# Optimization experiments

Measured on AMD Instinct MI355X. Metric: run time of the kernel, lower is better.

## Reference

```python
import jax, jax.numpy as jnp
import numpy as np

# Sizes derived from init_kwargs via calc_mlp_features:
# total_param=2117777, router_ratio=0.002 -> router_param=4235.554, expert_param=264192
# expert_hidden = 256, router_hidden = 352
N = 131072      # number of coordinate points
CIN = 3         # expert_insize == router_insize (xyz coords)
E = 8           # num_experts
K = 2           # top_k
H = 256         # expert_hidden (also SIREN data_channel)
RH = 352        # router_hidden
NHID = 3        # expert_layers - 2 hidden SIREN layers
W0C = 30.0      # sine frequency w0


def setup_inputs() -> dict:
    key = jax.random.key(0)
    ks = jax.random.split(key, 16)
    u = lambda k, shape, a: jax.random.uniform(k, shape, jnp.float32, -a, a)
    x = jax.random.uniform(ks[0], (N, CIN), jnp.float32, -1.0, 1.0)
    context = jax.random.uniform(ks[1], (N, CIN), jnp.float32, -1.0, 1.0)
    # Router: kaiming-normal weights, torch-default uniform biases
    Wr1 = jax.random.normal(ks[2], (CIN, RH), jnp.float32) * np.float32(np.sqrt(2.0 / CIN))
    br1 = u(ks[3], (RH,), 1.0 / np.sqrt(CIN))
    Wr2 = jax.random.normal(ks[4], (RH, E), jnp.float32) * np.float32(np.sqrt(2.0 / RH))
    br2 = u(ks[5], (E,), 1.0 / np.sqrt(RH))
    # SIREN experts (stacked over E): first layer U(-1/in, 1/in), rest U(+-sqrt(6/in)/30)
    sb = np.sqrt(6.0 / H) / 30.0
    W0 = u(ks[6], (E, CIN, H), 1.0 / CIN)
    b0 = u(ks[7], (E, H), 1.0 / np.sqrt(CIN))
    Wh = u(ks[8], (E, NHID, H, H), sb)
    bh = u(ks[9], (E, NHID, H), 1.0 / np.sqrt(H))
    Wo = u(ks[10], (E, H, H), sb)
    bo = u(ks[11], (E, H), 1.0 / np.sqrt(H))
    # Decoder: Linear(H,H)+ReLU+Linear(H,1)
    Wd1 = jax.random.normal(ks[12], (H, H), jnp.float32) * np.float32(np.sqrt(2.0 / H))
    bd1 = u(ks[13], (H,), 1.0 / np.sqrt(H))
    Wd2 = jax.random.normal(ks[14], (H, 1), jnp.float32) * np.float32(np.sqrt(2.0 / H))
    bd2 = u(ks[15], (1,), 1.0 / np.sqrt(H))
    return dict(x=x, context=context, Wr1=Wr1, br1=br1, Wr2=Wr2, br2=br2,
                W0=W0, b0=b0, Wh=Wh, bh=bh, Wo=Wo, bo=bo,
                Wd1=Wd1, bd1=bd1, Wd2=Wd2, bd2=bd2)


def reference(x, context, Wr1, br1, Wr2, br2, W0, b0, Wh, bh, Wo, bo, Wd1, bd1, Wd2, bd2):
    n = x.shape[0]
    # --- NoisyTopkRouter (eval path: no noise) ---
    logits = jnp.maximum(context @ Wr1 + br1, 0.0) @ Wr2 + br2          # [N, E]
    topv, topi = jax.lax.top_k(logits, K)                                # [N, K]
    # softmax over -inf-filled sparse logits == softmax over the top-k values
    w = jax.nn.softmax(topv, axis=-1)                                    # [N, K]
    gating = jnp.zeros_like(logits).at[jnp.arange(n)[:, None], topi].set(w)  # [N, E], zero off top-k
    # --- Per-expert SIREN, weighted combine ---
    # Masked dispatch + scatter-add in the original equals dense weighted sum
    # because gating is exactly zero for non-selected experts.
    def expert_step(acc, p):
        W0e, b0e, Whe, bhe, Woe, boe, ge = p
        h = jnp.sin(W0C * (x @ W0e + b0e))                # [N, H]
        for i in range(NHID):
            h = jnp.sin(W0C * (h @ Whe[i] + bhe[i]))
        out = h @ Woe + boe                               # [N, H], no output activation
        return acc + out * ge[:, None], None
    acc0 = jnp.zeros((n, H), dtype=x.dtype)
    final, _ = jax.lax.scan(expert_step, acc0, (W0, b0, Wh, bh, Wo, bo, gating.T))
    # --- Decoder ---
    return jnp.maximum(final @ Wd1 + bd1, 0.0) @ Wd2 + bd2               # [N, 1]
```

## Files before the change

kernel.cpp:

```cpp
#include <hip/hip_runtime.h>
#include <stdint.h>

#define N_PTS 131072
#define RH    352
#define BM    256
#define BME   64
#define TPB   512
#define SREV  4.774648292756860f

typedef short  bf16x8 __attribute__((ext_vector_type(8)));
typedef float  f32x16 __attribute__((ext_vector_type(16)));

__device__ __forceinline__ unsigned short f2bf(float f) {
  uint32_t u = __builtin_bit_cast(uint32_t, f);
  u = (u + 0x7FFFu + ((u >> 16) & 1u)) >> 16;
  return (unsigned short)u;
}
__device__ __forceinline__ float bf2f(unsigned short s) {
  return __builtin_bit_cast(float, ((uint32_t)s) << 16);
}
__device__ __forceinline__ float vsin1(float x) {
  float xf = x - floorf(x);
  float r;
  asm("v_sin_f32 %0, %1" : "=v"(r) : "v"(xf));
  return r;
}
__device__ __forceinline__ void ldsload16(const void* g, void* ldsWaveBase) {
  typedef __attribute__((address_space(3))) uint8_t lds_b;
  typedef __attribute__((address_space(1))) uint8_t glob_b;
  __builtin_amdgcn_global_load_lds((const glob_b*)g, (lds_b*)ldsWaveBase, 16, 0, 0);
}
__device__ __forceinline__ f32x16 mfma_bf16(bf16x8 a, bf16x8 b, f32x16 c) {
  return __builtin_amdgcn_mfma_f32_32x32x16_bf16(a, b, c, 0, 0, 0);
}

#define AWLOAD(d0, d1, addr64) \
  asm volatile("global_load_dwordx4 %0, %2, off\n\t" \
               "global_load_dwordx4 %1, %2, off offset:1024" \
               : "=&v"(d0), "=&v"(d1) : "v"(addr64))

#define VWAIT(N, r0, r1) \
  asm volatile("s_waitcnt vmcnt(" #N ")" : "+v"(r0), "+v"(r1))

__global__ __launch_bounds__(512) void pack_kernel(
    const float* __restrict__ W0, const float* __restrict__ b0,
    const float* __restrict__ Wh, const float* __restrict__ bh,
    const float* __restrict__ Wo, const float* __restrict__ bo,
    const float* __restrict__ Wd1, const float* __restrict__ bd1,
    short* __restrict__ pW0, short* __restrict__ pWh,
    short* __restrict__ pWo, short* __restrict__ pWd1)
{
  int b = blockIdx.x, tid = threadIdx.x;
  int jb = tid >> 6, l = tid & 63;
  int j  = jb*32 + (l & 31);
  int s0 = (l >> 5) * 8;
  unsigned short o[8];
  short* dp;

  if (b < 544) {
    int m = b / 17, slice = b % 17;
    int e = m >> 2, t = m & 3;
    const float* src; const float* bias; float scale; short* dst;
    if (t < 3) { src = Wh + (size_t)(e*3+t)*65536; bias = bh + (size_t)(e*3+t)*256; scale = SREV; dst = pWh + (size_t)(e*3+t)*69632; }
    else       { src = Wo + (size_t)e*65536;       bias = bo + (size_t)e*256;       scale = 1.0f; dst = pWo + (size_t)e*69632; }
    if (slice < 16) {
      #pragma unroll
      for (int i = 0; i < 8; ++i) {
        int k = slice*16 + s0 + i;
        o[i] = f2bf(scale * src[(size_t)k*256 + j]);
      }
    } else {
      #pragma unroll
      for (int i = 0; i < 8; ++i) o[i] = 0;
      if (s0 == 0) {
        float a = scale * bias[j];
        unsigned short h = f2bf(a);
        o[0] = h; o[1] = f2bf(a - bf2f(h));
      }
    }
    dp = dst + (size_t)slice*4096 + jb*512 + l*8;
  } else if (b < 552) {
    int e = b - 544;
    const float* w0 = W0 + (size_t)e*768;
    const float* bb = b0 + (size_t)e*256;
    #pragma unroll
    for (int i = 0; i < 8; ++i) {
      int s = s0 + i;
      unsigned short v = 0;
      if (s < 3) v = f2bf(SREV * w0[(size_t)s*256 + j]);
      else if (s < 6) { float a = SREV * w0[(size_t)(s-3)*256 + j]; unsigned short h = f2bf(a); v = f2bf(a - bf2f(h)); }
      else if (s < 9) v = f2bf(SREV * w0[(size_t)(s-6)*256 + j]);
      else if (s == 9)  v = f2bf(SREV * bb[j]);
      else if (s == 10) { float a = SREV * bb[j]; unsigned short h = f2bf(a); v = f2bf(a - bf2f(h)); }
      o[i] = v;
    }
    dp = pW0 + (size_t)e*4096 + jb*512 + l*8;
  } else {
    int slice = b - 552;
    if (slice < 16) {
      #pragma unroll
      for (int i = 0; i < 8; ++i) {
        int k = slice*16 + s0 + i;
        o[i] = f2bf(Wd1[(size_t)k*256 + j]);
      }
    } else {
      #pragma unroll
      for (int i = 0; i < 8; ++i) o[i] = 0;
      if (s0 == 0) {
        float a = bd1[j];
        unsigned short h = f2bf(a);
        o[0] = h; o[1] = f2bf(a - bf2f(h));
      }
    }
    dp = pWd1 + (size_t)slice*4096 + jb*512 + l*8;
  }
  uint4 v;
  v.x = (uint32_t)o[0] | ((uint32_t)o[1] << 16);
  v.y = (uint32_t)o[2] | ((uint32_t)o[3] << 16);
  v.z = (uint32_t)o[4] | ((uint32_t)o[5] << 16);
  v.w = (uint32_t)o[6] | ((uint32_t)o[7] << 16);
  *(uint4*)dp = v;
}

__global__ __launch_bounds__(256) void router_kernel(
    const float* __restrict__ ctx, const float* __restrict__ Wr1,
    const float* __restrict__ br1, const float* __restrict__ Wr2,
    const float* __restrict__ br2, uint4* __restrict__ topk,
    uint32_t* __restrict__ counts)
{
  __shared__ double w1d[RH*4];
  __shared__ double w2d[RH*8];
  __shared__ uint32_t lcnt[8];
  int tid = threadIdx.x;
  for (int i = tid; i < RH; i += 256) {
    w1d[i*4+0] = (double)Wr1[i];
    w1d[i*4+1] = (double)Wr1[352 + i];
    w1d[i*4+2] = (double)Wr1[704 + i];
    w1d[i*4+3] = (double)br1[i];
  }
  for (int i = tid; i < RH*8; i += 256) w2d[i] = (double)Wr2[i];
  if (tid < 8) lcnt[tid] = 0;
  __syncthreads();

  int n = blockIdx.x*256 + tid;
  double c0 = (double)ctx[(size_t)n*3+0];
  double c1 = (double)ctx[(size_t)n*3+1];
  double c2 = (double)ctx[(size_t)n*3+2];
  double lg[8];
  #pragma unroll
  for (int e = 0; e < 8; ++e) lg[e] = (double)br2[e];
  for (int j = 0; j < RH; ++j) {
    const double* a = &w1d[j*4];
    double h = c0*a[0] + c1*a[1] + c2*a[2] + a[3];
    h = h > 0.0 ? h : 0.0;
    const double* bq = &w2d[j*8];
    lg[0] += h*bq[0]; lg[1] += h*bq[1]; lg[2] += h*bq[2]; lg[3] += h*bq[3];
    lg[4] += h*bq[4]; lg[5] += h*bq[5]; lg[6] += h*bq[6]; lg[7] += h*bq[7];
  }
  double v0 = -1e300, v1 = -1e300; int i0 = 0, i1 = 0;
  #pragma unroll
  for (int e = 0; e < 8; ++e) {
    double lv = lg[e];
    if (lv > v0)      { v1 = v0; i1 = i0; v0 = lv; i0 = e; }
    else if (lv > v1) { v1 = lv; i1 = e; }
  }
  float ex = __expf((float)(v1 - v0));
  float s = 1.0f / (1.0f + ex);
  uint4 t;
  t.x = (uint32_t)i0 | ((uint32_t)i1 << 8);
  t.y = __builtin_bit_cast(uint32_t, s);
  t.z = __builtin_bit_cast(uint32_t, ex * s);
  t.w = 0;
  topk[n] = t;
  atomicAdd(&lcnt[i0], 1u); atomicAdd(&lcnt[i1], 1u);
  __syncthreads();
  if (tid < 8) atomicAdd(&counts[tid], lcnt[tid]);
}

__global__ void scan_kernel(const uint32_t* __restrict__ counts,
                            uint32_t* __restrict__ offsets,
                            uint32_t* __restrict__ cursors)
{
  if (threadIdx.x == 0) {
    uint32_t o = 0;
    for (int e = 0; e < 8; ++e) { offsets[e] = o; cursors[e] = o; o += counts[e]; }
    offsets[8] = o;
  }
}

__global__ __launch_bounds__(256) void scatter_kernel(
    const uint4* __restrict__ topk, uint32_t* __restrict__ cursors,
    uint32_t* __restrict__ plist, float* __restrict__ pw)
{
  __shared__ uint32_t lc[8], lb[8];
  int tid = threadIdx.x;
  if (tid < 8) lc[tid] = 0;
  __syncthreads();
  int n = blockIdx.x*256 + tid;
  uint4 t = topk[n];
  uint32_t e0 = t.x & 255u, e1 = (t.x >> 8) & 255u;
  uint32_t p0 = atomicAdd(&lc[e0], 1u);
  uint32_t p1 = atomicAdd(&lc[e1], 1u);
  __syncthreads();
  if (tid < 8) lb[tid] = atomicAdd(&cursors[tid], lc[tid]);
  __syncthreads();
  uint32_t d0 = lb[e0] + p0, d1 = lb[e1] + p1;
  plist[d0] = ((uint32_t)n << 1);      pw[d0] = __builtin_bit_cast(float, t.y);
  plist[d1] = ((uint32_t)n << 1) | 1u; pw[d1] = __builtin_bit_cast(float, t.z);
}

__global__ __launch_bounds__(256, 3) void expert_kernel(
    const float* __restrict__ x, const uint32_t* __restrict__ counts,
    const uint32_t* __restrict__ offsets, const uint32_t* __restrict__ plist,
    const float* __restrict__ pw, const short* __restrict__ pW0,
    const short* __restrict__ pWh, const short* __restrict__ pWo,
    short* __restrict__ outbuf)
{
  __shared__ __align__(16) uint8_t smem[34816];
  uint8_t* hB = smem;
  uint8_t* xB = smem + 32768;

  int tid = threadIdx.x;
  int lane = tid & 63;
  int jq = tid >> 6;
  int aoff = jq*2048 + lane*16;

  bf16x8 bbias;
  #pragma unroll
  for (int i = 0; i < 8; ++i) bbias[i] = 0;
  if (lane < 32) { bbias[0] = (short)0x3F80; bbias[1] = (short)0x3F80; }

  bf16x8 aw[5][2];
  f32x16 acc[2][2];

  int rr = tid >> 2;
  int rq = tid & 3;

  uint32_t tt = blockIdx.x;
  int e = -1; uint32_t cnt = 0;
  #pragma unroll 1
  for (int ee = 0; ee < 8; ++ee) {
    uint32_t c = counts[ee];
    uint32_t nt = (c + (BME-1)) >> 6;
    if (tt < nt) { e = ee; cnt = c; break; }
    tt -= nt;
  }
  if (e < 0) return;
  uint32_t base = offsets[e] + (tt << 6);
  int nvalid = (int)cnt - (int)(tt << 6); if (nvalid > BME) nvalid = BME;

  uint64_t matp[4];
  matp[0] = (uint64_t)(uintptr_t)(pWh + (size_t)(e*3+0)*69632);
  matp[1] = (uint64_t)(uintptr_t)(pWh + (size_t)(e*3+1)*69632);
  matp[2] = (uint64_t)(uintptr_t)(pWh + (size_t)(e*3+2)*69632);
  matp[3] = (uint64_t)(uintptr_t)(pWo + (size_t)e*69632);

  {
    uint64_t pb = matp[0] + (uint64_t)aoff;
    AWLOAD(aw[0][0], aw[0][1], pb);
    AWLOAD(aw[1][0], aw[1][1], pb + 8192);
    AWLOAD(aw[2][0], aw[2][1], pb + 16384);
    AWLOAD(aw[3][0], aw[3][1], pb + 24576);
  }

  float wgt[2];
  #pragma unroll
  for (int c = 0; c < 2; ++c) {
    int n = c*32 + (lane & 31);
    wgt[c] = (n < nvalid) ? pw[base + n] : 0.0f;
  }
  uint32_t psv = (rr < nvalid) ? plist[base + rr] : 0u;

  if (tid < BME) {
    float x0 = 0.0f, x1 = 0.0f, x2 = 0.0f;
    if (tid < nvalid) {
      uint32_t v = plist[base + tid];
      const float* xp = x + (size_t)(v >> 1)*3;
      x0 = xp[0]; x1 = xp[1]; x2 = xp[2];
    }
    unsigned short h0 = f2bf(x0), h1 = f2bf(x1), h2 = f2bf(x2);
    unsigned short l0 = f2bf(x0 - bf2f(h0)), l1 = f2bf(x1 - bf2f(h1)), l2 = f2bf(x2 - bf2f(h2));
    uint4 r0, r1;
    r0.x = (uint32_t)h0 | ((uint32_t)h1 << 16);
    r0.y = (uint32_t)h2 | ((uint32_t)h0 << 16);
    r0.z = (uint32_t)h1 | ((uint32_t)h2 << 16);
    r0.w = (uint32_t)l0 | ((uint32_t)l1 << 16);
    r1.x = (uint32_t)l2 | (0x3F80u << 16);
    r1.y = 0x3F80u;
    r1.z = 0u; r1.w = 0u;
    uint4* dst = (uint4*)(xB + tid*32);
    dst[0] = r0; dst[1] = r1;
  }

  const uint8_t* pw0e = (const uint8_t*)(pW0 + (size_t)e*4096);
  bf16x8 a0[2];
  a0[0] = *(const bf16x8*)(pw0e + aoff);
  a0[1] = *(const bf16x8*)(pw0e + aoff + 1024);

  __syncthreads();

  #pragma unroll
  for (int a2 = 0; a2 < 2; ++a2)
    #pragma unroll
    for (int c = 0; c < 2; ++c)
      #pragma unroll
      for (int r = 0; r < 16; ++r) acc[a2][c][r] = 0.0f;

  {
    bf16x8 bv[2];
    #pragma unroll
    for (int c = 0; c < 2; ++c) {
      int n = c*32 + (lane & 31);
      bv[c] = *(const bf16x8*)(xB + n*32 + ((lane >> 5)*16));
    }
    #pragma unroll
    for (int a2 = 0; a2 < 2; ++a2)
      #pragma unroll
      for (int c = 0; c < 2; ++c)
        acc[a2][c] = mfma_bf16(a0[a2], bv[c], acc[a2][c]);
  }

  #pragma unroll
  for (int a2 = 0; a2 < 2; ++a2) {
    int jb = jq*2 + a2;
    #pragma unroll
    for (int c = 0; c < 2; ++c) {
      int n = c*32 + (lane & 31);
      uint32_t rowb = (uint32_t)n * 512u;
      uint32_t sw = (uint32_t)((n & 7) << 4);
      #pragma unroll
      for (int g = 0; g < 4; ++g) {
        float s0f = vsin1(acc[a2][c][g*4+0]);
        float s1f = vsin1(acc[a2][c][g*4+1]);
        float s2f = vsin1(acc[a2][c][g*4+2]);
        float s3f = vsin1(acc[a2][c][g*4+3]);
        uint2 pv;
        pv.x = (uint32_t)f2bf(s0f) | ((uint32_t)f2bf(s1f) << 16);
        pv.y = (uint32_t)f2bf(s2f) | ((uint32_t)f2bf(s3f) << 16);
        int j0 = jb*32 + g*8 + ((lane >> 5) << 2);
        uint32_t off = (rowb + (uint32_t)(j0*2)) ^ sw;
        *(uint2*)(hB + off) = pv;
      }
    }
  }
  __syncthreads();

#define STEP(L, kb) { \
    enum { u_ = (L)*17 + (kb), ps_ = u_ + 4, us_ = u_ % 5, pss_ = ps_ % 5 }; \
    if (ps_ <= 67) { \
      uint64_t pa_ = matp[ps_/17] + (uint64_t)((ps_%17)*8192) + (uint64_t)aoff; \
      AWLOAD(aw[pss_][0], aw[pss_][1], pa_); \
    } \
    if (u_ <= 63)      { VWAIT(8, aw[us_][0], aw[us_][1]); } \
    else if (u_ == 64) { VWAIT(6, aw[us_][0], aw[us_][1]); } \
    else if (u_ == 65) { VWAIT(4, aw[us_][0], aw[us_][1]); } \
    else if (u_ == 66) { VWAIT(2, aw[us_][0], aw[us_][1]); } \
    else               { VWAIT(0, aw[us_][0], aw[us_][1]); } \
    bf16x8 bv0_, bv1_; \
    if ((kb) < 16) { \
      { int n_ = (lane & 31); \
        uint32_t off_ = ((uint32_t)n_*512u + (uint32_t)((kb)*32) + (uint32_t)((lane >> 5)*16)) \
                        ^ (uint32_t)((n_ & 7) << 4); \
        bv0_ = *(const bf16x8*)(hB + off_); } \
      { int n_ = 32 + (lane & 31); \
        uint32_t off_ = ((uint32_t)n_*512u + (uint32_t)((kb)*32) + (uint32_t)((lane >> 5)*16)) \
                        ^ (uint32_t)((n_ & 7) << 4); \
        bv1_ = *(const bf16x8*)(hB + off_); } \
    } else { bv0_ = bbias; bv1_ = bbias; } \
    acc[0][0] = mfma_bf16(aw[us_][0], bv0_, acc[0][0]); \
    acc[1][0] = mfma_bf16(aw[us_][1], bv0_, acc[1][0]); \
    acc[0][1] = mfma_bf16(aw[us_][0], bv1_, acc[0][1]); \
    acc[1][1] = mfma_bf16(aw[us_][1], bv1_, acc[1][1]); \
}
#define LAYER17(L) STEP(L,0) STEP(L,1) STEP(L,2) STEP(L,3) STEP(L,4) STEP(L,5) \
    STEP(L,6) STEP(L,7) STEP(L,8) STEP(L,9) STEP(L,10) STEP(L,11) STEP(L,12) \
    STEP(L,13) STEP(L,14) STEP(L,15) STEP(L,16)

#define ZACC() { _Pragma("unroll") for (int a2 = 0; a2 < 2; ++a2) \
    _Pragma("unroll") for (int c = 0; c < 2; ++c) \
    _Pragma("unroll") for (int r = 0; r < 16; ++r) acc[a2][c][r] = 0.0f; }

#define WRITE_SIN() { _Pragma("unroll") \
    for (int a2 = 0; a2 < 2; ++a2) { \
      int jb = jq*2 + a2; \
      _Pragma("unroll") \
      for (int c = 0; c < 2; ++c) { \
        int n = c*32 + (lane & 31); \
        uint32_t rowb = (uint32_t)n * 512u; \
        uint32_t sw = (uint32_t)((n & 7) << 4); \
        _Pragma("unroll") \
        for (int g = 0; g < 4; ++g) { \
          float s0f = vsin1(acc[a2][c][g*4+0]); \
          float s1f = vsin1(acc[a2][c][g*4+1]); \
          float s2f = vsin1(acc[a2][c][g*4+2]); \
          float s3f = vsin1(acc[a2][c][g*4+3]); \
          uint2 pv; \
          pv.x = (uint32_t)f2bf(s0f) | ((uint32_t)f2bf(s1f) << 16); \
          pv.y = (uint32_t)f2bf(s2f) | ((uint32_t)f2bf(s3f) << 16); \
          int j0 = jb*32 + g*8 + ((lane >> 5) << 2); \
          uint32_t off = (rowb + (uint32_t)(j0*2)) ^ sw; \
          *(uint2*)(hB + off) = pv; \
        } \
      } \
    } }

  ZACC(); LAYER17(0)
  __syncthreads(); WRITE_SIN(); __syncthreads();
  ZACC(); LAYER17(1)
  __syncthreads(); WRITE_SIN(); __syncthreads();
  ZACC(); LAYER17(2)
  __syncthreads(); WRITE_SIN(); __syncthreads();
  ZACC(); LAYER17(3)
  __syncthreads();
  #pragma unroll
  for (int a2 = 0; a2 < 2; ++a2) {
    int jb = jq*2 + a2;
    #pragma unroll
    for (int c = 0; c < 2; ++c) {
      int n = c*32 + (lane & 31);
      float w = wgt[c];
      uint32_t rowb = (uint32_t)n * 512u;
      uint32_t sw = (uint32_t)((n & 7) << 4);
      #pragma unroll
      for (int g = 0; g < 4; ++g) {
        float s0f = acc[a2][c][g*4+0] * w;
        float s1f = acc[a2][c][g*4+1] * w;
        float s2f = acc[a2][c][g*4+2] * w;
        float s3f = acc[a2][c][g*4+3] * w;
        uint2 pv;
        pv.x = (uint32_t)f2bf(s0f) | ((uint32_t)f2bf(s1f) << 16);
        pv.y = (uint32_t)f2bf(s2f) | ((uint32_t)f2bf(s3f) << 16);
        int j0 = jb*32 + g*8 + ((lane >> 5) << 2);
        uint32_t off = (rowb + (uint32_t)(j0*2)) ^ sw;
        *(uint2*)(hB + off) = pv;
      }
    }
  }
  __syncthreads();
  if (rr < nvalid) {
    uint4* dst = (uint4*)(outbuf + ((size_t)(psv & 1)*N_PTS + (size_t)(psv >> 1))*256);
    uint32_t rowb = (uint32_t)rr*512u;
    uint32_t sw = (uint32_t)((rr & 7) << 4);
    #pragma unroll
    for (int c = 0; c < 8; ++c) {
      int ch = c*4 + rq;
      dst[ch] = *(const uint4*)(hB + ((rowb + (uint32_t)(ch*16)) ^ sw));
    }
  }
}

#define LDS_DEC 150528

__global__ __launch_bounds__(TPB, 2) void decoder_kernel(
    const short* __restrict__ outbuf, const short* __restrict__ pWd1,
    const float* __restrict__ Wd2v, const float* __restrict__ bd2,
    float* __restrict__ outp)
{
  extern __shared__ __align__(16) uint8_t smem[];
  uint8_t* hB = smem;
  uint8_t* wB = smem + 131072;
  float* wd2 = (float*)(smem + 147456);
  float* part = (float*)(smem + 148480);

  int tid = threadIdx.x;
  int lane = tid & 63;
  int wv = tid >> 6;
  int nw = wv & 3;
  int jw = wv >> 2;
  int tbase = blockIdx.x * BM;

  ldsload16((const uint8_t*)pWd1 + (size_t)tid*16, wB + (tid >> 6)*1024);
  if (tid < 256) wd2[tid] = Wd2v[tid];

  const short* o0 = outbuf + (size_t)tbase*256;
  const short* o1 = outbuf + ((size_t)N_PTS + tbase)*256;
  #pragma unroll 1
  for (int it = 0; it < 16; ++it) {
    int c = it*512 + tid;
    uint4 a  = *(const uint4*)(o0 + (size_t)c*8);
    uint4 bq = *(const uint4*)(o1 + (size_t)c*8);
    uint4 ov;
    uint32_t* ap = (uint32_t*)&a;
    uint32_t* bp = (uint32_t*)&bq;
    uint32_t* op = (uint32_t*)&ov;
    #pragma unroll
    for (int w = 0; w < 4; ++w) {
      uint32_t ua = ap[w], ub = bp[w];
      float f0 = bf2f((unsigned short)(ua & 0xFFFFu)) + bf2f((unsigned short)(ub & 0xFFFFu));
      float f1 = bf2f((unsigned short)(ua >> 16))     + bf2f((unsigned short)(ub >> 16));
      op[w] = (uint32_t)f2bf(f0) | ((uint32_t)f2bf(f1) << 16);
    }
    int n = c >> 5;
    uint32_t off = ((uint32_t)n*512u + (uint32_t)(c & 31)*16u) ^ (uint32_t)((n & 7) << 4);
    *(uint4*)(hB + off) = ov;
  }
  __syncthreads();

  f32x16 acc[4][2];
  #pragma unroll
  for (int a2 = 0; a2 < 4; ++a2)
    #pragma unroll
    for (int c = 0; c < 2; ++c)
      #pragma unroll
      for (int r = 0; r < 16; ++r) acc[a2][c][r] = 0.0f;
  bf16x8 bbias;
  #pragma unroll
  for (int i = 0; i < 8; ++i) bbias[i] = 0;
  if (lane < 32) { bbias[0] = (short)0x3F80; bbias[1] = (short)0x3F80; }

  #pragma unroll 1
  for (int kb = 0; kb < 17; ++kb) {
    if (kb < 16)
      ldsload16((const uint8_t*)(pWd1 + (size_t)(kb+1)*4096) + (size_t)tid*16,
                wB + ((kb+1) & 1)*8192 + (tid >> 6)*1024);
    const uint8_t* wcur = wB + (kb & 1)*8192;
    bf16x8 av[4];
    #pragma unroll
    for (int a2 = 0; a2 < 4; ++a2)
      av[a2] = *(const bf16x8*)(wcur + (jw*4 + a2)*1024 + lane*16);
    bf16x8 bv[2];
    if (kb < 16) {
      #pragma unroll
      for (int c = 0; c < 2; ++c) {
        int n = (nw*2 + c)*32 + (lane & 31);
        uint32_t off = ((uint32_t)n*512u + (uint32_t)kb*32u + (uint32_t)((lane >> 5)*16))
                       ^ (uint32_t)((n & 7) << 4);
        bv[c] = *(const bf16x8*)(hB + off);
      }
    } else {
      bv[0] = bbias; bv[1] = bbias;
    }
    #pragma unroll
    for (int a2 = 0; a2 < 4; ++a2)
      #pragma unroll
      for (int c = 0; c < 2; ++c)
        acc[a2][c] = mfma_bf16(av[a2], bv[c], acc[a2][c]);
    __syncthreads();
  }

  float p0 = 0.0f, p1 = 0.0f;
  #pragma unroll
  for (int a2 = 0; a2 < 4; ++a2) {
    int jb = jw*4 + a2;
    #pragma unroll
    for (int c = 0; c < 2; ++c) {
      #pragma unroll
      for (int r = 0; r < 16; ++r) {
        int j = jb*32 + (r & 3) + ((r >> 2) << 3) + ((lane >> 5) << 2);
        float v = acc[a2][c][r];
        v = v > 0.0f ? v : 0.0f;
        float t = v * wd2[j];
        if (c == 0) p0 += t; else p1 += t;
      }
    }
  }
  p0 += __shfl_xor(p0, 32);
  p1 += __shfl_xor(p1, 32);
  if (lane < 32) {
    part[jw*256 + (nw*2+0)*32 + lane] = p0;
    part[jw*256 + (nw*2+1)*32 + lane] = p1;
  }
  __syncthreads();
  if (tid < 256)
    outp[tbase + tid] = part[tid] + part[256 + tid] + bd2[0];
}

extern "C" void kernel_launch(void* const* d_in, const int* in_sizes, int n_in,
                              void* d_out, int out_size, void* d_ws, size_t ws_size,
                              hipStream_t stream) {
  const float* x   = (const float*)d_in[0];
  const float* ctx = (const float*)d_in[1];
  const float* Wr1 = (const float*)d_in[2];
  const float* br1 = (const float*)d_in[3];
  const float* Wr2 = (const float*)d_in[4];
  const float* br2 = (const float*)d_in[5];
  const float* W0  = (const float*)d_in[6];
  const float* b0  = (const float*)d_in[7];
  const float* Wh  = (const float*)d_in[8];
  const float* bh  = (const float*)d_in[9];
  const float* Wo  = (const float*)d_in[10];
  const float* bo  = (const float*)d_in[11];
  const float* Wd1 = (const float*)d_in[12];
  const float* bd1 = (const float*)d_in[13];
  const float* Wd2 = (const float*)d_in[14];
  const float* bd2 = (const float*)d_in[15];
  float* out = (float*)d_out;

  const size_t WS_COUNTS  = 0;
  const size_t WS_CURSORS = 256;
  const size_t WS_OFFSETS = 512;
  const size_t WS_TOPK    = 1024;
  const size_t WS_PLIST   = WS_TOPK  + (size_t)N_PTS*16;
  const size_t WS_PW      = WS_PLIST + (size_t)N_PTS*8;
  const size_t WS_PW0     = WS_PW    + (size_t)N_PTS*8;
  const size_t WS_PWH     = WS_PW0   + (size_t)8*8192;
  const size_t WS_PWO     = WS_PWH   + (size_t)24*139264;
  const size_t WS_PWD1    = WS_PWO   + (size_t)8*139264;
  const size_t WS_OUT     = WS_PWD1  + (size_t)139264;
  const size_t WS_END     = WS_OUT   + (size_t)2*N_PTS*256*2;

  if (ws_size < WS_END) {
    hipMemsetAsync(d_out, 0xFF, (size_t)out_size*4, stream);
    return;
  }

  uint8_t* ws = (uint8_t*)d_ws;
  uint32_t* counts  = (uint32_t*)(ws + WS_COUNTS);
  uint32_t* cursors = (uint32_t*)(ws + WS_CURSORS);
  uint32_t* offsets = (uint32_t*)(ws + WS_OFFSETS);
  uint4*    topk    = (uint4*)   (ws + WS_TOPK);
  uint32_t* plist   = (uint32_t*)(ws + WS_PLIST);
  float*    pw      = (float*)   (ws + WS_PW);
  short*    pW0     = (short*)   (ws + WS_PW0);
  short*    pWh     = (short*)   (ws + WS_PWH);
  short*    pWo     = (short*)   (ws + WS_PWO);
  short*    pWd1    = (short*)   (ws + WS_PWD1);
  short*    outbuf  = (short*)   (ws + WS_OUT);

  hipMemsetAsync(counts, 0, 32, stream);
  hipFuncSetAttribute((const void*)decoder_kernel,
                      hipFuncAttributeMaxDynamicSharedMemorySize, LDS_DEC);

  pack_kernel   <<<569,  512, 0, stream>>>(W0, b0, Wh, bh, Wo, bo, Wd1, bd1,
                                           pW0, pWh, pWo, pWd1);
  router_kernel <<<512,  256, 0, stream>>>(ctx, Wr1, br1, Wr2, br2, topk, counts);
  scan_kernel   <<<1,     64, 0, stream>>>(counts, offsets, cursors);
  scatter_kernel<<<512,  256, 0, stream>>>(topk, cursors, plist, pw);
  expert_kernel <<<4104, 256, 0, stream>>>(x, counts, offsets, plist, pw,
                                           pW0, pWh, pWo, outbuf);
  decoder_kernel<<<512,  TPB, LDS_DEC, stream>>>(outbuf, pWd1, Wd2, bd2, out);
}
```

Baseline: 275.4 us.

## Double-buffer expert hidden activations in LDS to drop per-layer barrier

Splits the expert kernel's LDS activation tile into two ping-pong buffers, so each layer reads one buffer and writes its sine output into the other. This removes the extra __syncthreads that previously separated the last read of a layer from the overwrite. The output copy is also changed so each thread writes a contiguous 128-byte chunk of a row. In exchange, LDS per block roughly doubles and launch bounds drop from 3 to 2 blocks per CU, which reduces occupancy.

```diff
diff --git a/kernel.cpp b/kernel.cpp
--- a/kernel.cpp
+++ b/kernel.cpp
@@ -209,16 +209,19 @@
   plist[d1] = ((uint32_t)n << 1) | 1u; pw[d1] = __builtin_bit_cast(float, t.z);
 }
 
-__global__ __launch_bounds__(256, 3) void expert_kernel(
+#define LDS_EXPERT 67584
+
+__global__ __launch_bounds__(256, 2) void expert_kernel(
     const float* __restrict__ x, const uint32_t* __restrict__ counts,
     const uint32_t* __restrict__ offsets, const uint32_t* __restrict__ plist,
     const float* __restrict__ pw, const short* __restrict__ pW0,
     const short* __restrict__ pWh, const short* __restrict__ pWo,
     short* __restrict__ outbuf)
 {
-  __shared__ __align__(16) uint8_t smem[34816];
-  uint8_t* hB = smem;
-  uint8_t* xB = smem + 32768;
+  extern __shared__ __align__(16) uint8_t smem[];
+  uint8_t* hB0 = smem;
+  uint8_t* hB1 = smem + 32768;
+  uint8_t* xB  = smem + 65536;
 
   int tid = threadIdx.x;
   int lane = tid & 63;
@@ -320,67 +323,7 @@
         acc[a2][c] = mfma_bf16(a0[a2], bv[c], acc[a2][c]);
   }
 
-  #pragma unroll
-  for (int a2 = 0; a2 < 2; ++a2) {
-    int jb = jq*2 + a2;
-    #pragma unroll
-    for (int c = 0; c < 2; ++c) {
-      int n = c*32 + (lane & 31);
-      uint32_t rowb = (uint32_t)n * 512u;
-      uint32_t sw = (uint32_t)((n & 7) << 4);
-      #pragma unroll
-      for (int g = 0; g < 4; ++g) {
-        float s0f = vsin1(acc[a2][c][g*4+0]);
-        float s1f = vsin1(acc[a2][c][g*4+1]);
-        float s2f = vsin1(acc[a2][c][g*4+2]);
-        float s3f = vsin1(acc[a2][c][g*4+3]);
-        uint2 pv;
-        pv.x = (uint32_t)f2bf(s0f) | ((uint32_t)f2bf(s1f) << 16);
-        pv.y = (uint32_t)f2bf(s2f) | ((uint32_t)f2bf(s3f) << 16);
-        int j0 = jb*32 + g*8 + ((lane >> 5) << 2);
-        uint32_t off = (rowb + (uint32_t)(j0*2)) ^ sw;
-        *(uint2*)(hB + off) = pv;
-      }
-    }
-  }
-  __syncthreads();
-
-#define STEP(L, kb) { \
-    enum { u_ = (L)*17 + (kb), ps_ = u_ + 4, us_ = u_ % 5, pss_ = ps_ % 5 }; \
-    if (ps_ <= 67) { \
-      uint64_t pa_ = matp[ps_/17] + (uint64_t)((ps_%17)*8192) + (uint64_t)aoff; \
-      AWLOAD(aw[pss_][0], aw[pss_][1], pa_); \
-    } \
-    if (u_ <= 63)      { VWAIT(8, aw[us_][0], aw[us_][1]); } \
-    else if (u_ == 64) { VWAIT(6, aw[us_][0], aw[us_][1]); } \
-    else if (u_ == 65) { VWAIT(4, aw[us_][0], aw[us_][1]); } \
-    else if (u_ == 66) { VWAIT(2, aw[us_][0], aw[us_][1]); } \
-    else               { VWAIT(0, aw[us_][0], aw[us_][1]); } \
-    bf16x8 bv0_, bv1_; \
-    if ((kb) < 16) { \
-      { int n_ = (lane & 31); \
-        uint32_t off_ = ((uint32_t)n_*512u + (uint32_t)((kb)*32) + (uint32_t)((lane >> 5)*16)) \
-                        ^ (uint32_t)((n_ & 7) << 4); \
-        bv0_ = *(const bf16x8*)(hB + off_); } \
-      { int n_ = 32 + (lane & 31); \
-        uint32_t off_ = ((uint32_t)n_*512u + (uint32_t)((kb)*32) + (uint32_t)((lane >> 5)*16)) \
-                        ^ (uint32_t)((n_ & 7) << 4); \
-        bv1_ = *(const bf16x8*)(hB + off_); } \
-    } else { bv0_ = bbias; bv1_ = bbias; } \
-    acc[0][0] = mfma_bf16(aw[us_][0], bv0_, acc[0][0]); \
-    acc[1][0] = mfma_bf16(aw[us_][1], bv0_, acc[1][0]); \
-    acc[0][1] = mfma_bf16(aw[us_][0], bv1_, acc[0][1]); \
-    acc[1][1] = mfma_bf16(aw[us_][1], bv1_, acc[1][1]); \
-}
-#define LAYER17(L) STEP(L,0) STEP(L,1) STEP(L,2) STEP(L,3) STEP(L,4) STEP(L,5) \
-    STEP(L,6) STEP(L,7) STEP(L,8) STEP(L,9) STEP(L,10) STEP(L,11) STEP(L,12) \
-    STEP(L,13) STEP(L,14) STEP(L,15) STEP(L,16)
-
-#define ZACC() { _Pragma("unroll") for (int a2 = 0; a2 < 2; ++a2) \
-    _Pragma("unroll") for (int c = 0; c < 2; ++c) \
-    _Pragma("unroll") for (int r = 0; r < 16; ++r) acc[a2][c][r] = 0.0f; }
-
-#define WRITE_SIN() { _Pragma("unroll") \
+#define WRITE_SIN(HB) { _Pragma("unroll") \
     for (int a2 = 0; a2 < 2; ++a2) { \
       int jb = jq*2 + a2; \
       _Pragma("unroll") \
@@ -399,19 +342,54 @@
           pv.y = (uint32_t)f2bf(s2f) | ((uint32_t)f2bf(s3f) << 16); \
           int j0 = jb*32 + g*8 + ((lane >> 5) << 2); \
           uint32_t off = (rowb + (uint32_t)(j0*2)) ^ sw; \
-          *(uint2*)(hB + off) = pv; \
+          *(uint2*)((HB) + off) = pv; \
         } \
       } \
     } }
 
-  ZACC(); LAYER17(0)
-  __syncthreads(); WRITE_SIN(); __syncthreads();
-  ZACC(); LAYER17(1)
-  __syncthreads(); WRITE_SIN(); __syncthreads();
-  ZACC(); LAYER17(2)
-  __syncthreads(); WRITE_SIN(); __syncthreads();
-  ZACC(); LAYER17(3)
-  __syncthreads();
+  WRITE_SIN(hB0);
+  __syncthreads();
+
+#define STEP(L, kb, HB) { \
+    enum { u_ = (L)*17 + (kb), ps_ = u_ + 4, us_ = u_ % 5, pss_ = ps_ % 5 }; \
+    if (ps_ <= 67) { \
+      uint64_t pa_ = matp[ps_/17] + (uint64_t)((ps_%17)*8192) + (uint64_t)aoff; \
+      AWLOAD(aw[pss_][0], aw[pss_][1], pa_); \
+    } \
+    if (u_ <= 63)      { VWAIT(8, aw[us_][0], aw[us_][1]); } \
+    else if (u_ == 64) { VWAIT(6, aw[us_][0], aw[us_][1]); } \
+    else if (u_ == 65) { VWAIT(4, aw[us_][0], aw[us_][1]); } \
+    else if (u_ == 66) { VWAIT(2, aw[us_][0], aw[us_][1]); } \
+    else               { VWAIT(0, aw[us_][0], aw[us_][1]); } \
+    bf16x8 bv0_, bv1_; \
+    if ((kb) < 16) { \
+      { int n_ = (lane & 31); \
+        uint32_t off_ = ((uint32_t)n_*512u + (uint32_t)((kb)*32) + (uint32_t)((lane >> 5)*16)) \
+                        ^ (uint32_t)((n_ & 7) << 4); \
+        bv0_ = *(const bf16x8*)((HB) + off_); } \
+      { int n_ = 32 + (lane & 31); \
+        uint32_t off_ = ((uint32_t)n_*512u + (uint32_t)((kb)*32) + (uint32_t)((lane >> 5)*16)) \
+                        ^ (uint32_t)((n_ & 7) << 4); \
+        bv1_ = *(const bf16x8*)((HB) + off_); } \
+    } else { bv0_ = bbias; bv1_ = bbias; } \
+    acc[0][0] = mfma_bf16(aw[us_][0], bv0_, acc[0][0]); \
+    acc[1][0] = mfma_bf16(aw[us_][1], bv0_, acc[1][0]); \
+    acc[0][1] = mfma_bf16(aw[us_][0], bv1_, acc[0][1]); \
+    acc[1][1] = mfma_bf16(aw[us_][1], bv1_, acc[1][1]); \
+}
+#define LAYER17(L, HB) STEP(L,0,HB) STEP(L,1,HB) STEP(L,2,HB) STEP(L,3,HB) \
+    STEP(L,4,HB) STEP(L,5,HB) STEP(L,6,HB) STEP(L,7,HB) STEP(L,8,HB) \
+    STEP(L,9,HB) STEP(L,10,HB) STEP(L,11,HB) STEP(L,12,HB) STEP(L,13,HB) \
+    STEP(L,14,HB) STEP(L,15,HB) STEP(L,16,HB)
+
+#define ZACC() { _Pragma("unroll") for (int a2 = 0; a2 < 2; ++a2) \
+    _Pragma("unroll") for (int c = 0; c < 2; ++c) \
+    _Pragma("unroll") for (int r = 0; r < 16; ++r) acc[a2][c][r] = 0.0f; }
+
+  ZACC(); LAYER17(0, hB0) WRITE_SIN(hB1); __syncthreads();
+  ZACC(); LAYER17(1, hB1) WRITE_SIN(hB0); __syncthreads();
+  ZACC(); LAYER17(2, hB0) WRITE_SIN(hB1); __syncthreads();
+  ZACC(); LAYER17(3, hB1)
   #pragma unroll
   for (int a2 = 0; a2 < 2; ++a2) {
     int jb = jq*2 + a2;
@@ -432,20 +410,19 @@
         pv.y = (uint32_t)f2bf(s2f) | ((uint32_t)f2bf(s3f) << 16);
         int j0 = jb*32 + g*8 + ((lane >> 5) << 2);
         uint32_t off = (rowb + (uint32_t)(j0*2)) ^ sw;
-        *(uint2*)(hB + off) = pv;
+        *(uint2*)(hB0 + off) = pv;
       }
     }
   }
   __syncthreads();
   if (rr < nvalid) {
-    uint4* dst = (uint4*)(outbuf + ((size_t)(psv & 1)*N_PTS + (size_t)(psv >> 1))*256);
-    uint32_t rowb = (uint32_t)rr*512u;
+    uint4* dst = (uint4*)(outbuf + ((size_t)(psv & 1)*N_PTS + (size_t)(psv >> 1))*256
+                          + rq*64);
+    uint32_t rowb = (uint32_t)rr*512u + (uint32_t)rq*128u;
     uint32_t sw = (uint32_t)((rr & 7) << 4);
     #pragma unroll
-    for (int c = 0; c < 8; ++c) {
-      int ch = c*4 + rq;
-      dst[ch] = *(const uint4*)(hB + ((rowb + (uint32_t)(ch*16)) ^ sw));
-    }
+    for (int c = 0; c < 8; ++c)
+      dst[c] = *(const uint4*)(hB0 + ((rowb + (uint32_t)(c*16)) ^ sw));
   }
 }
 
@@ -618,6 +595,8 @@
   short*    outbuf  = (short*)   (ws + WS_OUT);
 
   hipMemsetAsync(counts, 0, 32, stream);
+  hipFuncSetAttribute((const void*)expert_kernel,
+                      hipFuncAttributeMaxDynamicSharedMemorySize, LDS_EXPERT);
   hipFuncSetAttribute((const void*)decoder_kernel,
                       hipFuncAttributeMaxDynamicSharedMemorySize, LDS_DEC);
 
@@ -626,7 +605,7 @@
   router_kernel <<<512,  256, 0, stream>>>(ctx, Wr1, br1, Wr2, br2, topk, counts);
   scan_kernel   <<<1,     64, 0, stream>>>(counts, offsets, cursors);
   scatter_kernel<<<512,  256, 0, stream>>>(topk, cursors, plist, pw);
-  expert_kernel <<<4104, 256, 0, stream>>>(x, counts, offsets, plist, pw,
-                                           pW0, pWh, pWo, outbuf);
+  expert_kernel <<<4104, 256, LDS_EXPERT, stream>>>(x, counts, offsets, plist, pw,
+                                                    pW0, pWh, pWo, outbuf);
   decoder_kernel<<<512,  TPB, LDS_DEC, stream>>>(outbuf, pWd1, Wd2, bd2, out);
 }
```

Measured after the change: 277.7 us. About the same (+0.8%).
